# Performance work log

Measured on AMD Instinct MI355X. Metric: run time of the kernel, lower is better.

## Reference

```python
import jax, jax.numpy as jnp
import numpy as np

INIT_STD = 0.002
DEFAULT_BETA = 1.0 / np.sqrt(64.0)  # 1/sqrt(head_dim)


def setup_inputs() -> dict:
    key = jax.random.key(0)
    k1, k2, k3 = jax.random.split(key, 3)
    B, S, E = 4, 2048, 768
    H, D = 12, 64
    x = jax.random.normal(k1, (B, S, E), dtype=jnp.float32)
    q_proj_weight = INIT_STD * jax.random.normal(k2, (H, D, E), dtype=jnp.float32)
    k_proj_weight = INIT_STD * jax.random.normal(k3, (H, D, E), dtype=jnp.float32)
    beta = jnp.full((H,), DEFAULT_BETA, dtype=jnp.float32)
    return {"x": x, "q_proj_weight": q_proj_weight, "k_proj_weight": k_proj_weight, "beta": beta}


def reference(x, q_proj_weight, k_proj_weight, beta):
    # x: [B,S,E]; W^{Q,K}: [H,D,E]; beta: [H]
    q = jnp.einsum("bse,hde->bshd", x, q_proj_weight)  # [B,S,H,D]
    k = jnp.einsum("bse,hde->bshd", x, k_proj_weight)  # [B,S,H,D]
    # scores[b,h,s,t] = beta_h * <Q_{bsh}, K_{bth}>
    scores = jnp.einsum("bshd,bthd,h->bhst", q, k, beta)
    S = x.shape[1]
    diag = jnp.eye(S, dtype=bool)  # self-exclusion mask (B != C)
    scores = jnp.where(diag[None, None, :, :], -jnp.inf, scores)
    lse = jax.nn.logsumexp(scores, axis=-1)  # [B,H,S]
    # E = -sum_{b,h,s} (1/beta_h) * logsumexp_t
    energy = -jnp.sum(lse / beta[None, :, None])
    return energy
```

## Files before the change

### kernel.cpp

```cpp
#include <hip/hip_runtime.h>
#include <hip/hip_bf16.h>

typedef __attribute__((ext_vector_type(8))) short short8v;
typedef __attribute__((ext_vector_type(4))) float f32x4;

static constexpr int B_ = 4, S_ = 2048, E_ = 768, H_ = 12, D_ = 64;
static constexpr int NROWS = B_ * H_ * S_;
static constexpr float LOG2E = 1.44269504088896340736f;
static constexpr float LN2 = 0.69314718055994530942f;

typedef __attribute__((address_space(3))) unsigned int lds_u32;
typedef const __attribute__((address_space(1))) unsigned int glb_u32;

__device__ __forceinline__ void gload16(const void* g, void* l) {
  __builtin_amdgcn_global_load_lds((glb_u32*)g, (lds_u32*)l, 16, 0, 0);
}

#define VM0 asm volatile("s_waitcnt vmcnt(0)" ::: "memory")
#define VM2 asm volatile("s_waitcnt vmcnt(2)" ::: "memory")
#define BAR __builtin_amdgcn_s_barrier()

__device__ __forceinline__ unsigned short f2bf(float f) {
  union { float f; unsigned int u; } v; v.f = f;
  unsigned int u = v.u;
  unsigned int r = (u + 0x7fffu + ((u >> 16) & 1u)) >> 16;
  return (unsigned short)r;
}

__global__ __launch_bounds__(256) void cvt_w_kernel(const float4* __restrict__ wq,
                                                    const float4* __restrict__ wk,
                                                    const float* __restrict__ beta,
                                                    ushort4* __restrict__ wb, int n4) {
  int i = blockIdx.x * 256 + threadIdx.x;
  if (i < n4) {
    int row = i / (E_ / 4);
    float sc = beta[row >> 6] * LOG2E;
    float4 v = wq[i];
    ushort4 o;
    o.x = f2bf(v.x * sc); o.y = f2bf(v.y * sc); o.z = f2bf(v.z * sc); o.w = f2bf(v.w * sc);
    wb[i] = o;
  } else if (i < 2 * n4) {
    int j = i - n4;
    float4 v = wk[j];
    ushort4 o;
    o.x = f2bf(v.x); o.y = f2bf(v.y); o.z = f2bf(v.z); o.w = f2bf(v.w);
    wb[i] = o;
  }
}

__global__ __launch_bounds__(256) void proj_kernel(const float* __restrict__ x,
                                                   const unsigned short* __restrict__ wb,
                                                   unsigned short* __restrict__ Qb,
                                                   unsigned short* __restrict__ Kb) {
  __shared__ float lAf[128 * 32];
  __shared__ unsigned short lB[128 * 32];
  const int mt = blockIdx.x, nt = blockIdx.y;
  const int t = threadIdx.x;
  const int wid = t >> 6, lane = t & 63, l15 = lane & 15, lhi = lane >> 4;
  const int wr = (wid >> 1) * 64, wc = (wid & 1) * 64;

  f32x4 acc[4][4] = {};

  const int r3 = t >> 3;
  const int cs = (t & 7) ^ (r3 & 7);
  const float* gA = x + (size_t)(mt * 128 + r3) * E_ + cs * 4;

  const int row = t >> 2, ch = t & 3;
  const unsigned short* gB = wb + (size_t)(nt * 128 + row) * E_ + ch * 8;

  for (int k0 = 0; k0 < E_; k0 += 32) {
    gload16(gA + k0,                (char*)lAf + t * 16);
    gload16(gA + 32 * E_ + k0,      (char*)lAf + 4096 + t * 16);
    gload16(gA + 64 * E_ + k0,      (char*)lAf + 8192 + t * 16);
    gload16(gA + 96 * E_ + k0,      (char*)lAf + 12288 + t * 16);
    gload16(gB + k0,                &lB[t * 8]);
    gload16(gB + (size_t)64 * E_ + k0, &lB[2048 + t * 8]);
    __syncthreads();
    short8v aF[4], bF[4];
    const int sw_ = l15 & 7;
#pragma unroll
    for (int m = 0; m < 4; ++m) {
      const int r = wr + m * 16 + l15;
      const float* base = lAf + r * 32;
      f32x4 u0 = *(const f32x4*)(base + ((((lhi << 1)    ) ^ sw_) << 2));
      f32x4 u1 = *(const f32x4*)(base + ((((lhi << 1) | 1) ^ sw_) << 2));
      union { short8v s8; unsigned int u[4]; } af;
      asm("v_cvt_pk_bf16_f32 %0, %1, %2" : "=v"(af.u[0]) : "v"(u0[0]), "v"(u0[1]));
      asm("v_cvt_pk_bf16_f32 %0, %1, %2" : "=v"(af.u[1]) : "v"(u0[2]), "v"(u0[3]));
      asm("v_cvt_pk_bf16_f32 %0, %1, %2" : "=v"(af.u[2]) : "v"(u1[0]), "v"(u1[1]));
      asm("v_cvt_pk_bf16_f32 %0, %1, %2" : "=v"(af.u[3]) : "v"(u1[2]), "v"(u1[3]));
      aF[m] = af.s8;
    }
#pragma unroll
    for (int n = 0; n < 4; ++n)
      bF[n] = *(const short8v*)&lB[(wc + n * 16 + l15) * 32 + lhi * 8];
#pragma unroll
    for (int m = 0; m < 4; ++m)
#pragma unroll
      for (int n = 0; n < 4; ++n)
        acc[m][n] = __builtin_amdgcn_mfma_f32_16x16x32_bf16(aF[m], bF[n], acc[m][n], 0, 0, 0);
    __syncthreads();
  }

  const int nbase = nt * 128 + wc;
  unsigned short* dst = (nbase < 768) ? Qb : Kb;
  const int nb = (nbase < 768) ? nbase : nbase - 768;
#pragma unroll
  for (int m = 0; m < 4; ++m)
#pragma unroll
    for (int n = 0; n < 4; ++n)
#pragma unroll
      for (int r = 0; r < 4; ++r) {
        int M = mt * 128 + wr + m * 16 + lhi * 4 + r;
        int col = nb + n * 16 + l15;
        int h = col >> 6, d = col & 63;
        int b = M >> 11, s = M & (S_ - 1);
        dst[((((size_t)b * H_ + h) * S_ + s) << 6) + d] = f2bf(acc[m][n][r]);
      }
}

__device__ __forceinline__ void stageK(const unsigned short* __restrict__ Kbase, int t0,
                                       int tid, unsigned short* lbuf) {
  const int w = tid >> 6;
  const int r = tid >> 3;
  const int c = (tid & 7) ^ (r & 7);
  const char* src = (const char*)Kbase + ((size_t)(t0 + r) << 7) + (c << 4);
  char* ldst = (char*)lbuf + (w << 10);
  gload16(src, ldst);
  gload16(src + (32 << 7), ldst + 4096);
}

__device__ __forceinline__ void computeTile64(const unsigned short* lbuf, const short8v q[4][2],
                                              f32x4 sp[4], bool isD, int l15, int lhi) {
  short8v kf[4][2];
  const int sw = l15 & 7;
#pragma unroll
  for (int f = 0; f < 4; ++f) {
    const char* p = (const char*)lbuf + ((f * 16 + l15) << 7);
    kf[f][0] = *(const short8v*)(p + ((lhi ^ sw) << 4));
    kf[f][1] = *(const short8v*)(p + (((lhi + 4) ^ sw) << 4));
  }
#pragma unroll
  for (int rb = 0; rb < 4; ++rb) {
    f32x4 acc[4] = {};
#pragma unroll
    for (int f = 0; f < 4; ++f) {
      acc[f] = __builtin_amdgcn_mfma_f32_16x16x32_bf16(q[rb][0], kf[f][0], acc[f], 0, 0, 0);
      acc[f] = __builtin_amdgcn_mfma_f32_16x16x32_bf16(q[rb][1], kf[f][1], acc[f], 0, 0, 0);
    }
#pragma unroll
    for (int f = 0; f < 4; ++f) {
      f32x4 e;
#pragma unroll
      for (int r = 0; r < 4; ++r) e[r] = __builtin_amdgcn_exp2f(acc[f][r]);
      if (isD && f == rb) {
#pragma unroll
        for (int r = 0; r < 4; ++r)
          if (l15 == lhi * 4 + r) e[r] = 0.f;
      }
      sp[rb] += e;
    }
  }
}

__global__ __launch_bounds__(256) void lse_kernel(const unsigned short* __restrict__ Qb,
                                                  const unsigned short* __restrict__ Kb,
                                                  float* __restrict__ rowsum) {
  __shared__ __align__(16) unsigned short lK[3][4096];
  const int L = blockIdx.x + 8 * (blockIdx.y + 12 * blockIdx.z);
  const int xcd = L & 7, j = L >> 3;
  const int split = j & 3;
  const int st = (j >> 2) & 7;
  const int g = xcd + 8 * (j >> 5);
  const int h = g % H_, b = g / H_;

  const int tid = threadIdx.x;
  const int wid = tid >> 6, lane = tid & 63;
  const int l15 = lane & 15, lhi = lane >> 4;
  const size_t hb = ((size_t)b * H_ + h) * S_;
  const unsigned short* Qbase = Qb + hb * D_;
  const unsigned short* Kbase = Kb + hb * D_;
  const int s0 = st * 256 + wid * 64;
  const int tb = split * 512;

  short8v q[4][2];
#pragma unroll
  for (int rb = 0; rb < 4; ++rb) {
    const unsigned short* qr = Qbase + (size_t)(s0 + rb * 16 + l15) * D_ + lhi * 8;
    q[rb][0] = *(const short8v*)qr;
    q[rb][1] = *(const short8v*)(qr + 32);
  }

  const int dtile = ((s0 >> 9) == split) ? ((s0 - tb) >> 6) : -1;

  f32x4 sp[4] = {};
  stageK(Kbase, tb, tid, lK[0]);
  stageK(Kbase, tb + 64, tid, lK[1]);
  int bi = 0;
#pragma unroll 1
  for (int i = 0; i < 7; ++i) {
    VM2;
    BAR;
    if (i < 6) {
      int bs_ = bi + 2; if (bs_ >= 3) bs_ -= 3;
      stageK(Kbase, tb + (i + 2) * 64, tid, lK[bs_]);
    }
    computeTile64(lK[bi], q, sp, i == dtile, l15, lhi);
    if (++bi == 3) bi = 0;
  }
  VM0; BAR;
  computeTile64(lK[bi], q, sp, 7 == dtile, l15, lhi);

#pragma unroll
  for (int rb = 0; rb < 4; ++rb)
#pragma unroll
    for (int r = 0; r < 4; ++r) {
      float s = sp[rb][r];
#pragma unroll
      for (int off = 1; off < 16; off <<= 1) s += __shfl_xor(s, off, 64);
      if (l15 == 0)
        rowsum[(size_t)split * NROWS + hb + s0 + rb * 16 + lhi * 4 + r] = s;
    }
}

__global__ __launch_bounds__(256) void finish1_kernel(const float* __restrict__ rowsum,
                                                      const float* __restrict__ beta,
                                                      float* __restrict__ partial) {
  int row = blockIdx.x * 256 + threadIdx.x;
  float s = (rowsum[row] + rowsum[NROWS + row]) +
            (rowsum[2 * NROWS + row] + rowsum[3 * NROWS + row]);
  int h = (row >> 11) % H_;
  float c = __builtin_amdgcn_logf(s) * LN2 / beta[h];
#pragma unroll
  for (int off = 1; off < 64; off <<= 1) c += __shfl_xor(c, off, 64);
  __shared__ float wsum[4];
  int wid = threadIdx.x >> 6;
  if ((threadIdx.x & 63) == 0) wsum[wid] = c;
  __syncthreads();
  if (threadIdx.x == 0) partial[blockIdx.x] = wsum[0] + wsum[1] + wsum[2] + wsum[3];
}

__global__ __launch_bounds__(256) void finish2_kernel(const float* __restrict__ partial, int n,
                                                      float* __restrict__ out) {
  float s = 0.f;
  for (int i = threadIdx.x; i < n; i += 256) s += partial[i];
#pragma unroll
  for (int off = 1; off < 64; off <<= 1) s += __shfl_xor(s, off, 64);
  __shared__ float wsum[4];
  int wid = threadIdx.x >> 6;
  if ((threadIdx.x & 63) == 0) wsum[wid] = s;
  __syncthreads();
  if (threadIdx.x == 0) out[0] = -(wsum[0] + wsum[1] + wsum[2] + wsum[3]);
}

extern "C" void kernel_launch(void* const* d_in, const int* in_sizes, int n_in,
                              void* d_out, int out_size, void* d_ws, size_t ws_size,
                              hipStream_t stream) {
  const float* x    = (const float*)d_in[0];
  const float* wq   = (const float*)d_in[1];
  const float* wk   = (const float*)d_in[2];
  const float* beta = (const float*)d_in[3];

  char* ws = (char*)d_ws;
  const size_t wb_bytes = (size_t)2 * H_ * D_ * E_ * 2;
  const size_t qk_bytes = (size_t)B_ * H_ * S_ * D_ * 2;
  const size_t rs_bytes = (size_t)4 * NROWS * 4;
  unsigned short* wb = (unsigned short*)ws;
  unsigned short* Qb = (unsigned short*)(ws + wb_bytes);
  unsigned short* Kb = (unsigned short*)(ws + wb_bytes + qk_bytes);
  float* rowsum      = (float*)(ws + wb_bytes + 2 * qk_bytes);
  float* partial     = (float*)(ws + wb_bytes + 2 * qk_bytes + rs_bytes);

  int nw4 = (H_ * D_ * E_) / 4;
  cvt_w_kernel<<<(2 * nw4 + 255) / 256, 256, 0, stream>>>((const float4*)wq, (const float4*)wk,
                                                          beta, (ushort4*)wb, nw4);

  dim3 pgrid((B_ * S_) / 128, (2 * H_ * D_) / 128);
  proj_kernel<<<pgrid, 256, 0, stream>>>(x, wb, Qb, Kb);

  dim3 lgrid(S_ / 256, H_, B_ * 4);
  lse_kernel<<<lgrid, 256, 0, stream>>>(Qb, Kb, rowsum);

  finish1_kernel<<<NROWS / 256, 256, 0, stream>>>(rowsum, beta, partial);
  finish2_kernel<<<1, 256, 0, stream>>>(partial, NROWS / 256, (float*)d_out);
}
```

Baseline: 77.92 us.

## Convert x tile to bf16 in registers before LDS, prefetch next tile, swizzle

The projection kernel now loads the fp32 x tile into registers, converts it to bf16 once, and stores it to LDS, instead of staging fp32 in LDS and converting per wave. The next k-step of x is prefetched into registers while the MFMAs run, and both A and B LDS tiles use an XOR swizzle on 16-byte chunks to avoid bank conflicts. This halves LDS footprint and traffic for A and removes redundant conversions done by multiple waves. The cost is more register pressure and hand-written waitcnt and barrier ordering that must stay correct.

```diff
diff --git a/kernel.cpp b/kernel.cpp
--- a/kernel.cpp
+++ b/kernel.cpp
@@ -18,6 +18,8 @@
 
 #define VM0 asm volatile("s_waitcnt vmcnt(0)" ::: "memory")
 #define VM2 asm volatile("s_waitcnt vmcnt(2)" ::: "memory")
+#define VM4 asm volatile("s_waitcnt vmcnt(4)" ::: "memory")
+#define LG0 asm volatile("s_waitcnt lgkmcnt(0)" ::: "memory")
 #define BAR __builtin_amdgcn_s_barrier()
 
 __device__ __forceinline__ unsigned short f2bf(float f) {
@@ -52,7 +54,7 @@
                                                    const unsigned short* __restrict__ wb,
                                                    unsigned short* __restrict__ Qb,
                                                    unsigned short* __restrict__ Kb) {
-  __shared__ float lAf[128 * 32];
+  __shared__ unsigned short lA[128 * 32];
   __shared__ unsigned short lB[128 * 32];
   const int mt = blockIdx.x, nt = blockIdx.y;
   const int t = threadIdx.x;
@@ -61,45 +63,60 @@
 
   f32x4 acc[4][4] = {};
 
-  const int r3 = t >> 3;
-  const int cs = (t & 7) ^ (r3 & 7);
-  const float* gA = x + (size_t)(mt * 128 + r3) * E_ + cs * 4;
-
   const int row = t >> 2, ch = t & 3;
-  const unsigned short* gB = wb + (size_t)(nt * 128 + row) * E_ + ch * 8;
+  const int chs = ch ^ (row & 3);
+  const float* gA = x + (size_t)(mt * 128 + row) * E_ + chs * 8;
+  const unsigned short* gB = wb + (size_t)(nt * 128 + row) * E_ + chs * 8;
+
+  f32x4 a0 = *(const f32x4*)(gA);
+  f32x4 a1 = *(const f32x4*)(gA + 4);
+  f32x4 a2 = *(const f32x4*)(gA + 64 * E_);
+  f32x4 a3 = *(const f32x4*)(gA + 64 * E_ + 4);
 
   for (int k0 = 0; k0 < E_; k0 += 32) {
-    gload16(gA + k0,                (char*)lAf + t * 16);
-    gload16(gA + 32 * E_ + k0,      (char*)lAf + 4096 + t * 16);
-    gload16(gA + 64 * E_ + k0,      (char*)lAf + 8192 + t * 16);
-    gload16(gA + 96 * E_ + k0,      (char*)lAf + 12288 + t * 16);
-    gload16(gB + k0,                &lB[t * 8]);
+    BAR;
+    gload16(gB + k0, &lB[t * 8]);
     gload16(gB + (size_t)64 * E_ + k0, &lB[2048 + t * 8]);
-    __syncthreads();
+    VM2;
+    union { short8v s8; unsigned int u[4]; } c0, c1;
+    asm("v_cvt_pk_bf16_f32 %0, %1, %2" : "=v"(c0.u[0]) : "v"(a0[0]), "v"(a0[1]));
+    asm("v_cvt_pk_bf16_f32 %0, %1, %2" : "=v"(c0.u[1]) : "v"(a0[2]), "v"(a0[3]));
+    asm("v_cvt_pk_bf16_f32 %0, %1, %2" : "=v"(c0.u[2]) : "v"(a1[0]), "v"(a1[1]));
+    asm("v_cvt_pk_bf16_f32 %0, %1, %2" : "=v"(c0.u[3]) : "v"(a1[2]), "v"(a1[3]));
+    asm("v_cvt_pk_bf16_f32 %0, %1, %2" : "=v"(c1.u[0]) : "v"(a2[0]), "v"(a2[1]));
+    asm("v_cvt_pk_bf16_f32 %0, %1, %2" : "=v"(c1.u[1]) : "v"(a2[2]), "v"(a2[3]));
+    asm("v_cvt_pk_bf16_f32 %0, %1, %2" : "=v"(c1.u[2]) : "v"(a3[0]), "v"(a3[1]));
+    asm("v_cvt_pk_bf16_f32 %0, %1, %2" : "=v"(c1.u[3]) : "v"(a3[2]), "v"(a3[3]));
+    *(short8v*)&lA[row * 32 + ch * 8] = c0.s8;
+    *(short8v*)&lA[(row + 64) * 32 + ch * 8] = c1.s8;
+    if (k0 + 32 < E_) {
+      a0 = *(const f32x4*)(gA + k0 + 32);
+      a1 = *(const f32x4*)(gA + k0 + 36);
+      a2 = *(const f32x4*)(gA + 64 * E_ + k0 + 32);
+      a3 = *(const f32x4*)(gA + 64 * E_ + k0 + 36);
+      LG0;
+      VM4;
+    } else {
+      LG0;
+      VM0;
+    }
+    BAR;
     short8v aF[4], bF[4];
-    const int sw_ = l15 & 7;
 #pragma unroll
     for (int m = 0; m < 4; ++m) {
       const int r = wr + m * 16 + l15;
-      const float* base = lAf + r * 32;
-      f32x4 u0 = *(const f32x4*)(base + ((((lhi << 1)    ) ^ sw_) << 2));
-      f32x4 u1 = *(const f32x4*)(base + ((((lhi << 1) | 1) ^ sw_) << 2));
-      union { short8v s8; unsigned int u[4]; } af;
-      asm("v_cvt_pk_bf16_f32 %0, %1, %2" : "=v"(af.u[0]) : "v"(u0[0]), "v"(u0[1]));
-      asm("v_cvt_pk_bf16_f32 %0, %1, %2" : "=v"(af.u[1]) : "v"(u0[2]), "v"(u0[3]));
-      asm("v_cvt_pk_bf16_f32 %0, %1, %2" : "=v"(af.u[2]) : "v"(u1[0]), "v"(u1[1]));
-      asm("v_cvt_pk_bf16_f32 %0, %1, %2" : "=v"(af.u[3]) : "v"(u1[2]), "v"(u1[3]));
-      aF[m] = af.s8;
-    }
-#pragma unroll
-    for (int n = 0; n < 4; ++n)
-      bF[n] = *(const short8v*)&lB[(wc + n * 16 + l15) * 32 + lhi * 8];
+      aF[m] = *(const short8v*)&lA[r * 32 + ((lhi ^ (l15 & 3)) << 3)];
+    }
+#pragma unroll
+    for (int n = 0; n < 4; ++n) {
+      const int r = wc + n * 16 + l15;
+      bF[n] = *(const short8v*)&lB[r * 32 + ((lhi ^ (l15 & 3)) << 3)];
+    }
 #pragma unroll
     for (int m = 0; m < 4; ++m)
 #pragma unroll
       for (int n = 0; n < 4; ++n)
         acc[m][n] = __builtin_amdgcn_mfma_f32_16x16x32_bf16(aF[m], bF[n], acc[m][n], 0, 0, 0);
-    __syncthreads();
   }
 
   const int nbase = nt * 128 + wc;
```

After: 76.28 us. 2.1% less time.
